# Optimization experiments

Measured on AMD Instinct MI355X. Metric: run time of the kernel, lower is better.

The kernel has to match this reference:

```python
import jax, jax.numpy as jnp
import numpy as np

N, E, G = 50000, 800000, 256
H, C = 8, 16
F0 = 64
FH = H * C  # 128
L = 6
EPS = 1e-5
SEL = [0, 1, 2, 3, 4, 5, 5, 5]  # <10 layers -> pad with last


def setup_inputs() -> dict:
    key = jax.random.key(0)
    ks = jax.random.split(key, 32)

    def w(k, shape, fan_in):
        return jax.random.normal(k, shape, jnp.float32) / np.float32(np.sqrt(fan_in))

    inp = {
        'x': jax.random.normal(ks[0], (N, F0), jnp.float32),
        'edge_index': jax.random.randint(ks[1], (2, E), 0, N),
        'batch_vec': jnp.sort(jax.random.randint(ks[2], (N,), 0, G)),
        # layer 0 (in=F0)
        'Wq0': w(ks[3], (F0, FH), F0), 'bq0': 0.01 * jax.random.normal(ks[4], (FH,), jnp.float32),
        'Wk0': w(ks[5], (F0, FH), F0), 'bk0': 0.01 * jax.random.normal(ks[6], (FH,), jnp.float32),
        'Wv0': w(ks[7], (F0, FH), F0), 'bv0': 0.01 * jax.random.normal(ks[8], (FH,), jnp.float32),
        'Ws0': w(ks[9], (F0, FH), F0), 'bs0': 0.01 * jax.random.normal(ks[10], (FH,), jnp.float32),
        # layers 1..L-1 (in=FH), stacked
        'Wq': w(ks[11], (L - 1, FH, FH), FH), 'bq': 0.01 * jax.random.normal(ks[12], (L - 1, FH), jnp.float32),
        'Wk': w(ks[13], (L - 1, FH, FH), FH), 'bk': 0.01 * jax.random.normal(ks[14], (L - 1, FH), jnp.float32),
        'Wv': w(ks[15], (L - 1, FH, FH), FH), 'bv': 0.01 * jax.random.normal(ks[16], (L - 1, FH), jnp.float32),
        'Ws': w(ks[17], (L - 1, FH, FH), FH), 'bs': 0.01 * jax.random.normal(ks[18], (L - 1, FH), jnp.float32),
        # BatchNorm affine params per layer
        'gamma': jnp.ones((L, FH), jnp.float32),
        'beta': jnp.zeros((L, FH), jnp.float32),
    }
    return inp


def _transformer_conv(x, src, dst, Wq, bq, Wk, bk, Wv, bv, Ws, bs):
    # q from target nodes, k/v from source nodes (PyG TransformerConv, concat=True)
    q = (x @ Wq + bq).reshape(-1, H, C)
    k = (x @ Wk + bk).reshape(-1, H, C)
    v = (x @ Wv + bv).reshape(-1, H, C)
    s = jnp.einsum('ehc,ehc->eh', q[dst], k[src]) * np.float32(1.0 / np.sqrt(C))  # [E,H]
    m = jax.ops.segment_max(s, dst, num_segments=N)       # segment softmax over in-edges
    e = jnp.exp(s - m[dst])
    denom = jax.ops.segment_sum(e, dst, num_segments=N)
    alpha = e / jnp.maximum(denom[dst], 1e-16)            # [E,H]
    msg = jax.ops.segment_sum(alpha[:, :, None] * v[src], dst, num_segments=N)  # [N,H,C]
    return msg.reshape(-1, FH) + (x @ Ws + bs)            # root/skip connection


def _bn_relu(x, g, b):
    mu = jnp.mean(x, axis=0)
    var = jnp.var(x, axis=0)  # biased, as used for normalization in training mode
    return jax.nn.relu((x - mu) * jax.lax.rsqrt(var + EPS) * g + b)


def reference(x, edge_index, batch_vec, Wq0, bq0, Wk0, bk0, Wv0, bv0, Ws0, bs0,
              Wq, bq, Wk, bk, Wv, bv, Ws, bs, gamma, beta):
    src, dst = edge_index[0], edge_index[1]
    outs = []
    h = _bn_relu(_transformer_conv(x, src, dst, Wq0, bq0, Wk0, bk0, Wv0, bv0, Ws0, bs0),
                 gamma[0], beta[0])
    outs.append(h)
    for i in range(L - 1):
        h = _bn_relu(_transformer_conv(h, src, dst, Wq[i], bq[i], Wk[i], bk[i],
                                       Wv[i], bv[i], Ws[i], bs[i]),
                     gamma[i + 1], beta[i + 1])
        outs.append(h)
    counts = jnp.maximum(jax.ops.segment_sum(jnp.ones((N,), x.dtype), batch_vec, num_segments=G), 1.0)
    pooled = [jax.ops.segment_sum(o, batch_vec, num_segments=G) / counts[:, None] for o in outs]
    latent = jnp.stack([pooled[i] for i in SEL], axis=1)  # [G, 8, FH]
    return latent.reshape(G, -1)                          # [G, 8*FH]
```

## Files before the change

### kernel.cpp

```cpp
#include <hip/hip_runtime.h>
#include <hip/hip_bf16.h>
#include <math.h>

#define NN 50000
#define NE 800000
#define NG 256
#define FHH 128
#define NL 6
#define NCH 49
#define NB 391

typedef __attribute__((ext_vector_type(8))) short s16x8;
typedef __attribute__((ext_vector_type(4))) float f32x4;

#define QSCALE 0.36067376022224085f

__device__ __forceinline__ ushort f2bf(float x) {
  uint u = __float_as_uint(x);
  u += 0x7fffu + ((u >> 16) & 1u);
  return (ushort)(u >> 16);
}
__device__ __forceinline__ float bf2f(ushort h) {
  return __uint_as_float(((uint)h) << 16);
}
__device__ __forceinline__ float bfl(uint u) { return __uint_as_float(u << 16); }
__device__ __forceinline__ float bfh(uint u) { return __uint_as_float(u & 0xffff0000u); }

__device__ __forceinline__ void gload16(const ushort* g, ushort* l) {
  __builtin_amdgcn_global_load_lds(
      (const __attribute__((address_space(1))) uint*)(const void*)g,
      (__attribute__((address_space(3))) uint*)(void*)l, 16, 0, 0);
}

__global__ void k_gstart(const int* __restrict__ bv, int* __restrict__ gstart) {
  int g = blockIdx.x * blockDim.x + threadIdx.x;
  if (g > NG) return;
  int lo = 0, hi = NN;
  while (lo < hi) { int mid = (lo + hi) >> 1; if (bv[mid] < g) lo = mid + 1; else hi = mid; }
  gstart[g] = lo;
}

__global__ void k_deg(const int* __restrict__ dstv, int* __restrict__ deg) {
  int e = blockIdx.x * blockDim.x + threadIdx.x;
  if (e < NE) atomicAdd(&deg[dstv[e]], 1);
}

__global__ __launch_bounds__(256) void k_scanA(const int* __restrict__ deg, int* __restrict__ part) {
  int b = blockIdx.x, t = threadIdx.x;
  int s = 0;
  for (int j = t; j < 1024; j += 256) { int i = b * 1024 + j; if (i < NN) s += deg[i]; }
  __shared__ int sh[4];
  for (int o = 32; o; o >>= 1) s += __shfl_down(s, o, 64);
  if ((t & 63) == 0) sh[t >> 6] = s;
  __syncthreads();
  if (t == 0) part[b] = sh[0] + sh[1] + sh[2] + sh[3];
}

__global__ void k_scanB(int* __restrict__ part, int* __restrict__ row_ptr) {
  if (threadIdx.x == 0 && blockIdx.x == 0) {
    int run = 0;
    for (int i = 0; i < NCH; ++i) { int v = part[i]; part[i] = run; run += v; }
    row_ptr[NN] = run;
  }
}

__global__ __launch_bounds__(1024) void k_scanC(const int* __restrict__ deg, const int* __restrict__ part,
                                                int* __restrict__ row_ptr, int* __restrict__ cursor) {
  __shared__ int buf[1024];
  int b = blockIdx.x, t = threadIdx.x;
  int i = b * 1024 + t;
  int v = (i < NN) ? deg[i] : 0;
  buf[t] = v;
  __syncthreads();
  for (int off = 1; off < 1024; off <<= 1) {
    int add = (t >= off) ? buf[t - off] : 0;
    __syncthreads();
    buf[t] += add;
    __syncthreads();
  }
  if (i < NN) { int ex = part[b] + buf[t] - v; row_ptr[i] = ex; cursor[i] = ex; }
}

__global__ void k_scatter(const int* __restrict__ srcv, const int* __restrict__ dstv,
                          int* __restrict__ cursor, uint* __restrict__ colb) {
  int e = blockIdx.x * blockDim.x + threadIdx.x;
  if (e < NE) {
    int d = dstv[e];
    int pos = atomicAdd(&cursor[d], 1);
    colb[pos] = ((uint)srcv[e]) << 9;
  }
}

__device__ __forceinline__ size_t wtile_idx(int k, int c) {
  return (size_t)(k >> 5) * 4096 + ((((c >> 4) * 4 + ((k & 31) >> 3)) * 16 + (c & 15)) * 8 + (k & 7));
}

__global__ __launch_bounds__(256) void k_wconv0(const float* __restrict__ W0, const float* __restrict__ W1,
                                                const float* __restrict__ W2, const float* __restrict__ W3,
                                                ushort* __restrict__ wh, ushort* __restrict__ wl) {
  int id = blockIdx.x * 256 + threadIdx.x;
  if (id >= 4 * 64 * 128) return;
  int mat = id >> 13, rem = id & 8191;
  int k = rem >> 7, c = rem & 127;
  const float* W = (mat == 0) ? W0 : (mat == 1) ? W1 : (mat == 2) ? W2 : W3;
  float v = W[k * 128 + c];
  ushort h = f2bf(v);
  ushort lo = f2bf(v - bf2f(h));
  size_t dst = (size_t)mat * 8192 + wtile_idx(k, c);
  wh[dst] = h; wl[dst] = lo;
}

__global__ __launch_bounds__(256) void k_wconvS(const float* __restrict__ Wq, const float* __restrict__ Wk,
                                                const float* __restrict__ Wv, const float* __restrict__ Ws,
                                                ushort* __restrict__ wh, ushort* __restrict__ wl) {
  int id = blockIdx.x * 256 + threadIdx.x;
  if (id >= 5 * 4 * 16384) return;
  int lay = id / 65536, rem = id % 65536;
  int mat = rem >> 14, rem2 = rem & 16383;
  int k = rem2 >> 7, c = rem2 & 127;
  const float* W = (mat == 0) ? Wq : (mat == 1) ? Wk : (mat == 2) ? Wv : Ws;
  float v = W[(size_t)lay * 16384 + k * 128 + c];
  ushort h = f2bf(v);
  ushort lo = f2bf(v - bf2f(h));
  size_t dst = 32768 + ((size_t)lay * 4 + mat) * 16384 + wtile_idx(k, c);
  wh[dst] = h; wl[dst] = lo;
}

template <int K>
__global__ __launch_bounds__(256) void k_presplit(const float* __restrict__ Y,
                                                  ushort* __restrict__ Xh, ushort* __restrict__ Xl) {
  const int CP = K / 4;
  int idx = blockIdx.x * 256 + threadIdx.x;
  int row = idx / CP;
  int c4 = (idx % CP) * 4;
  if (row >= NN) return;
  float4 v = *reinterpret_cast<const float4*>(Y + (size_t)row * K + c4);
  ushort h0 = f2bf(v.x), h1 = f2bf(v.y), h2 = f2bf(v.z), h3 = f2bf(v.w);
  ushort l0 = f2bf(v.x - bf2f(h0)), l1 = f2bf(v.y - bf2f(h1));
  ushort l2 = f2bf(v.z - bf2f(h2)), l3 = f2bf(v.w - bf2f(h3));
  int b = row >> 7, g = (row & 127) >> 4, frow = row & 15;
  int ks = c4 >> 5, qq = (c4 & 31) >> 3, j = c4 & 7;
  size_t base = ((size_t)ks * NB + b) * 4096 + (((g * 4 + qq) * 16) + frow) * 8 + j;
  *reinterpret_cast<uint2*>(Xh + base) =
      make_uint2((uint)h0 | ((uint)h1 << 16), (uint)h2 | ((uint)h3 << 16));
  *reinterpret_cast<uint2*>(Xl + base) =
      make_uint2((uint)l0 | ((uint)l1 << 16), (uint)l2 | ((uint)l3 << 16));
}

template <int K>
__global__ __launch_bounds__(256, 2) void k_gemm(
    const ushort* __restrict__ Xh, const ushort* __restrict__ Xl,
    const ushort* __restrict__ Wth, const ushort* __restrict__ Wtl,
    const float* __restrict__ b0, const float* __restrict__ b1,
    const float* __restrict__ b2, const float* __restrict__ b3,
    ushort* __restrict__ qbf, ushort* __restrict__ kv, float* __restrict__ Yxs) {
  __shared__ __align__(16) ushort Ah[4096];
  __shared__ __align__(16) ushort Al[4096];
  __shared__ __align__(16) ushort Bh[4096];
  __shared__ __align__(16) ushort Bl[4096];
  int t = threadIdx.x;
  int lane = t & 63, w = t >> 6;
  int wr = w >> 1, wc = w & 1;
  int frow = lane & 15;
  int mat = blockIdx.y;
  const ushort* wh = Wth + (size_t)mat * (K * 128);
  const ushort* wl = Wtl + (size_t)mat * (K * 128);
  const float* bb = (mat == 0) ? b0 : (mat == 1) ? b1 : (mat == 2) ? b2 : b3;

  f32x4 acc[4][4];
#pragma unroll
  for (int i = 0; i < 4; ++i)
#pragma unroll
    for (int j = 0; j < 4; ++j)
#pragma unroll
      for (int r = 0; r < 4; ++r) acc[i][j][r] = 0.f;

  int wofs = w * 1024 + lane * 8;
  for (int ks = 0; ks < K / 32; ++ks) {
    size_t abase = ((size_t)ks * NB + blockIdx.x) * 4096;
    const ushort* gAh = Xh + abase + wofs;
    const ushort* gAl = Xl + abase + wofs;
    const ushort* gBh = wh + ks * 4096 + wofs;
    const ushort* gBl = wl + ks * 4096 + wofs;
    gload16(gAh, &Ah[w * 1024]);
    gload16(gAh + 512, &Ah[w * 1024 + 512]);
    gload16(gAl, &Al[w * 1024]);
    gload16(gAl + 512, &Al[w * 1024 + 512]);
    gload16(gBh, &Bh[w * 1024]);
    gload16(gBh + 512, &Bh[w * 1024 + 512]);
    gload16(gBl, &Bl[w * 1024]);
    gload16(gBl + 512, &Bl[w * 1024 + 512]);
    __syncthreads();
    s16x8 ah[4], al[4], bh[4], bl[4];
#pragma unroll
    for (int g = 0; g < 4; ++g) {
      ah[g] = *reinterpret_cast<const s16x8*>(&Ah[(wr * 4 + g) * 512 + lane * 8]);
      al[g] = *reinterpret_cast<const s16x8*>(&Al[(wr * 4 + g) * 512 + lane * 8]);
      bh[g] = *reinterpret_cast<const s16x8*>(&Bh[(wc * 4 + g) * 512 + lane * 8]);
      bl[g] = *reinterpret_cast<const s16x8*>(&Bl[(wc * 4 + g) * 512 + lane * 8]);
    }
#pragma unroll
    for (int rg = 0; rg < 4; ++rg)
#pragma unroll
      for (int cg = 0; cg < 4; ++cg) {
        acc[rg][cg] = __builtin_amdgcn_mfma_f32_16x16x32_bf16(ah[rg], bh[cg], acc[rg][cg], 0, 0, 0);
        acc[rg][cg] = __builtin_amdgcn_mfma_f32_16x16x32_bf16(al[rg], bh[cg], acc[rg][cg], 0, 0, 0);
        acc[rg][cg] = __builtin_amdgcn_mfma_f32_16x16x32_bf16(ah[rg], bl[cg], acc[rg][cg], 0, 0, 0);
      }
    __syncthreads();
  }
  int r0 = blockIdx.x * 128;
  int qq = (lane >> 4) << 2;
#pragma unroll
  for (int rg = 0; rg < 4; ++rg) {
#pragma unroll
    for (int cg = 0; cg < 4; ++cg) {
      int colg = wc * 64 + cg * 16 + frow;
      float bv = bb[colg];
#pragma unroll
      for (int r = 0; r < 4; ++r) {
        int row = r0 + wr * 64 + rg * 16 + qq + r;
        if (row >= NN) continue;
        float val = acc[rg][cg][r] + bv;
        if (mat == 0)      qbf[(size_t)row * FHH + colg] = f2bf(val * QSCALE);
        else if (mat == 3) Yxs[(size_t)row * FHH + colg] = val;
        else {
          int pos = (colg >> 1) * 4 + ((mat == 2) ? 2 : 0) + (colg & 1);
          kv[(size_t)row * 256 + pos] = f2bf(val);
        }
      }
    }
  }
}

__global__ __launch_bounds__(256) void k_agg(const uint* __restrict__ qb,
                                             const ushort* __restrict__ kv,
                                             const float* __restrict__ xs,
                                             const int* __restrict__ row_ptr,
                                             const uint* __restrict__ colb,
                                             float* __restrict__ y) {
  int n = blockIdx.x * 4 + (threadIdx.x >> 6);
  int t = threadIdx.x & 63;
  uint qp = qb[(n << 6) + t];
  float qx = bfl(qp), qy = bfh(qp);
  const char* kvb = (const char*)kv;
  uint tof = (uint)t * 8u;
  int e0 = row_ptr[n], e1 = row_ptr[n + 1];
  float sum = 0.f, a0 = 0.f, a1 = 0.f;
  int i = e0;
  for (; i + 4 <= e1; i += 4) {
    uint o0 = colb[i] + tof, o1 = colb[i + 1] + tof;
    uint o2 = colb[i + 2] + tof, o3 = colb[i + 3] + tof;
    uint2 d0 = *(const uint2*)(kvb + o0);
    uint2 d1 = *(const uint2*)(kvb + o1);
    uint2 d2 = *(const uint2*)(kvb + o2);
    uint2 d3 = *(const uint2*)(kvb + o3);
    float p0 = fmaf(qx, bfl(d0.x), qy * bfh(d0.x));
    float p1 = fmaf(qx, bfl(d1.x), qy * bfh(d1.x));
    float p2 = fmaf(qx, bfl(d2.x), qy * bfh(d2.x));
    float p3 = fmaf(qx, bfl(d3.x), qy * bfh(d3.x));
    p0 += __shfl_xor(p0, 1, 8); p1 += __shfl_xor(p1, 1, 8);
    p2 += __shfl_xor(p2, 1, 8); p3 += __shfl_xor(p3, 1, 8);
    p0 += __shfl_xor(p0, 2, 8); p1 += __shfl_xor(p1, 2, 8);
    p2 += __shfl_xor(p2, 2, 8); p3 += __shfl_xor(p3, 2, 8);
    p0 += __shfl_xor(p0, 4, 8); p1 += __shfl_xor(p1, 4, 8);
    p2 += __shfl_xor(p2, 4, 8); p3 += __shfl_xor(p3, 4, 8);
    float w0 = exp2f(fminf(p0, 110.f));
    float w1 = exp2f(fminf(p1, 110.f));
    float w2 = exp2f(fminf(p2, 110.f));
    float w3 = exp2f(fminf(p3, 110.f));
    sum += (w0 + w1) + (w2 + w3);
    a0 = fmaf(w0, bfl(d0.y), fmaf(w1, bfl(d1.y), fmaf(w2, bfl(d2.y), fmaf(w3, bfl(d3.y), a0))));
    a1 = fmaf(w0, bfh(d0.y), fmaf(w1, bfh(d1.y), fmaf(w2, bfh(d2.y), fmaf(w3, bfh(d3.y), a1))));
  }
  for (; i < e1; ++i) {
    uint o0 = colb[i] + tof;
    uint2 d0 = *(const uint2*)(kvb + o0);
    float p0 = fmaf(qx, bfl(d0.x), qy * bfh(d0.x));
    p0 += __shfl_xor(p0, 1, 8);
    p0 += __shfl_xor(p0, 2, 8);
    p0 += __shfl_xor(p0, 4, 8);
    float w0 = exp2f(fminf(p0, 110.f));
    sum += w0;
    a0 = fmaf(w0, bfl(d0.y), a0);
    a1 = fmaf(w0, bfh(d0.y), a1);
  }
  float inv = 1.f / fmaxf(sum, 1e-16f);
  float2 xv = *reinterpret_cast<const float2*>(xs + ((size_t)n << 7) + 2 * t);
  float2 ov;
  ov.x = fmaf(a0, inv, xv.x);
  ov.y = fmaf(a1, inv, xv.y);
  *reinterpret_cast<float2*>(y + ((size_t)n << 7) + 2 * t) = ov;
}

__global__ __launch_bounds__(256) void k_bnstats(const float* __restrict__ y,
                                                 float* __restrict__ sums,
                                                 float* __restrict__ sumsq) {
  __shared__ float s1[256], s2[256];
  int f = threadIdx.x & 127;
  int half = threadIdx.x >> 7;
  float a = 0.f, b = 0.f;
  for (int r = blockIdx.x * 2 + half; r < NN; r += 512) {
    float val = y[(size_t)r * FHH + f];
    a += val;
    b += val * val;
  }
  s1[threadIdx.x] = a;
  s2[threadIdx.x] = b;
  __syncthreads();
  if (half == 0) {
    a += s1[threadIdx.x + 128];
    b += s2[threadIdx.x + 128];
    atomicAdd(&sums[f], a);
    atomicAdd(&sumsq[f], b);
  }
}

template <int WRITE_X>
__global__ __launch_bounds__(256) void k_post(const float* __restrict__ y,
                                              const float* __restrict__ sums,
                                              const float* __restrict__ sumsq,
                                              const float* __restrict__ gvec,
                                              const float* __restrict__ bvec_,
                                              const int* __restrict__ bv,
                                              const int* __restrict__ gstart,
                                              float* __restrict__ out, int layer,
                                              ushort* __restrict__ Xh, ushort* __restrict__ Xl) {
  __shared__ float acts[8][128];
  __shared__ int sg[8];
  __shared__ float ssc[128], ssh[128];
  int b = blockIdx.x, t = threadIdx.x;
  if (t < 128) {
    const float invn = 1.f / (float)NN;
    float mu = sums[t] * invn;
    float var = sumsq[t] * invn - mu * mu;
    float sc = gvec[t] * rsqrtf(var + 1e-5f);
    ssc[t] = sc;
    ssh[t] = bvec_[t] - mu * sc;
  }
  if (t < 8) sg[t] = (b * 8 + t < NN) ? bv[b * 8 + t] : -1;
  __syncthreads();
  int row = b * 8 + (t >> 5);
  int c4 = (t & 31) * 4;
  bool ok = row < NN;
  float4 a = make_float4(0.f, 0.f, 0.f, 0.f);
  if (ok) {
    float4 v = *reinterpret_cast<const float4*>(y + (size_t)row * FHH + c4);
    a.x = fmaxf(fmaf(v.x, ssc[c4 + 0], ssh[c4 + 0]), 0.f);
    a.y = fmaxf(fmaf(v.y, ssc[c4 + 1], ssh[c4 + 1]), 0.f);
    a.z = fmaxf(fmaf(v.z, ssc[c4 + 2], ssh[c4 + 2]), 0.f);
    a.w = fmaxf(fmaf(v.w, ssc[c4 + 3], ssh[c4 + 3]), 0.f);
  }
  *reinterpret_cast<float4*>(&acts[t >> 5][c4]) = a;
  if (WRITE_X && ok) {
    ushort h0 = f2bf(a.x), h1 = f2bf(a.y), h2 = f2bf(a.z), h3 = f2bf(a.w);
    ushort l0 = f2bf(a.x - bf2f(h0)), l1 = f2bf(a.y - bf2f(h1));
    ushort l2 = f2bf(a.z - bf2f(h2)), l3 = f2bf(a.w - bf2f(h3));
    int bb = row >> 7, g = (row & 127) >> 4, frow = row & 15;
    int ks = c4 >> 5, qq = (c4 & 31) >> 3, j = c4 & 7;
    size_t base = ((size_t)ks * NB + bb) * 4096 + (((g * 4 + qq) * 16) + frow) * 8 + j;
    *reinterpret_cast<uint2*>(Xh + base) =
        make_uint2((uint)h0 | ((uint)h1 << 16), (uint)h2 | ((uint)h3 << 16));
    *reinterpret_cast<uint2*>(Xl + base) =
        make_uint2((uint)l0 | ((uint)l1 << 16), (uint)l2 | ((uint)l3 << 16));
  }
  __syncthreads();
  if (t < 128) {
    float racc = 0.f;
    int cg = sg[0];
    for (int r = 0; r < 8; ++r) {
      int g = sg[r];
      if (g != cg) {
        if (cg >= 0) {
          float p = racc / (float)(gstart[cg + 1] - gstart[cg]);
          if (layer < 5) atomicAdd(&out[(size_t)cg * 1024 + layer * FHH + t], p);
          else {
            atomicAdd(&out[(size_t)cg * 1024 + 5 * FHH + t], p);
            atomicAdd(&out[(size_t)cg * 1024 + 6 * FHH + t], p);
            atomicAdd(&out[(size_t)cg * 1024 + 7 * FHH + t], p);
          }
        }
        racc = 0.f;
        cg = g;
      }
      racc += acts[r][t];
    }
    if (cg >= 0) {
      float p = racc / (float)(gstart[cg + 1] - gstart[cg]);
      if (layer < 5) atomicAdd(&out[(size_t)cg * 1024 + layer * FHH + t], p);
      else {
        atomicAdd(&out[(size_t)cg * 1024 + 5 * FHH + t], p);
        atomicAdd(&out[(size_t)cg * 1024 + 6 * FHH + t], p);
        atomicAdd(&out[(size_t)cg * 1024 + 7 * FHH + t], p);
      }
    }
  }
}

extern "C" void kernel_launch(void* const* d_in, const int* in_sizes, int n_in,
                              void* d_out, int out_size, void* d_ws, size_t ws_size,
                              hipStream_t stream) {
  (void)in_sizes; (void)n_in; (void)ws_size;
  const float* x    = (const float*)d_in[0];
  const int*   ei   = (const int*)d_in[1];
  const int*   bvec = (const int*)d_in[2];
  const float* Wq0  = (const float*)d_in[3];
  const float* bq0  = (const float*)d_in[4];
  const float* Wk0  = (const float*)d_in[5];
  const float* bk0  = (const float*)d_in[6];
  const float* Wv0  = (const float*)d_in[7];
  const float* bv0  = (const float*)d_in[8];
  const float* Ws0  = (const float*)d_in[9];
  const float* bs0  = (const float*)d_in[10];
  const float* WqS  = (const float*)d_in[11];
  const float* bqS  = (const float*)d_in[12];
  const float* WkS  = (const float*)d_in[13];
  const float* bkS  = (const float*)d_in[14];
  const float* WvS  = (const float*)d_in[15];
  const float* bvS  = (const float*)d_in[16];
  const float* WsS  = (const float*)d_in[17];
  const float* bsS  = (const float*)d_in[18];
  const float* gamma = (const float*)d_in[19];
  const float* beta  = (const float*)d_in[20];
  float* out = (float*)d_out;

  char* ws = (char*)d_ws;
  size_t off = 0;
  auto alloc = [&](size_t bytes) {
    void* p = ws + off;
    off = (off + bytes + 255) & ~(size_t)255;
    return p;
  };
  ushort* qbf = (ushort*)alloc((size_t)NN * FHH * 2);
  float* xs   = (float*)alloc((size_t)NN * FHH * 4);
  float* y    = (float*)alloc((size_t)NN * FHH * 4);
  ushort* kv  = (ushort*)alloc((size_t)NN * 256 * 2);
  ushort* Xh  = (ushort*)alloc((size_t)4 * NB * 4096 * 2 + 8192);
  ushort* Xl  = (ushort*)alloc((size_t)4 * NB * 4096 * 2 + 8192);
  uint* colb   = (uint*)alloc((size_t)NE * 4);
  int* row_ptr = (int*)alloc((size_t)(NN + 1) * 4);
  int* cursor  = (int*)alloc((size_t)NN * 4);
  int* deg     = (int*)alloc((size_t)NN * 4);
  int* part    = (int*)alloc((size_t)NCH * 4);
  int* gstart  = (int*)alloc((size_t)(NG + 1) * 4);
  float* bstat = (float*)alloc((size_t)NL * 2 * FHH * 4);
  ushort* wsh = (ushort*)alloc((size_t)360448 * 2);
  ushort* wsl = (ushort*)alloc((size_t)360448 * 2);

  const int* srcv = ei;
  const int* dstv = ei + NE;

  hipMemsetAsync(out, 0, (size_t)out_size * 4, stream);
  hipMemsetAsync(deg, 0, (size_t)NN * 4, stream);
  hipMemsetAsync(bstat, 0, (size_t)NL * 2 * FHH * 4, stream);
  k_gstart<<<5, 64, 0, stream>>>(bvec, gstart);
  k_deg<<<(NE + 255) / 256, 256, 0, stream>>>(dstv, deg);
  k_scanA<<<NCH, 256, 0, stream>>>(deg, part);
  k_scanB<<<1, 64, 0, stream>>>(part, row_ptr);
  k_scanC<<<NCH, 1024, 0, stream>>>(deg, part, row_ptr, cursor);
  k_scatter<<<(NE + 255) / 256, 256, 0, stream>>>(srcv, dstv, cursor, colb);
  k_wconv0<<<128, 256, 0, stream>>>(Wq0, Wk0, Wv0, Ws0, wsh, wsl);
  k_wconvS<<<1280, 256, 0, stream>>>(WqS, WkS, WvS, WsS, wsh, wsl);
  k_presplit<64><<<(NN * 16 + 255) / 256, 256, 0, stream>>>(x, Xh, Xl);

  for (int l = 0; l < NL; ++l) {
    const ushort* WthL = wsh + ((l == 0) ? 0 : (size_t)32768 + (size_t)(l - 1) * 65536);
    const ushort* WtlL = wsl + ((l == 0) ? 0 : (size_t)32768 + (size_t)(l - 1) * 65536);
    const float *bq_, *bk_, *bv_, *bs_;
    if (l == 0) { bq_ = bq0; bk_ = bk0; bv_ = bv0; bs_ = bs0; }
    else {
      size_t bo = (size_t)(l - 1) * FHH;
      bq_ = bqS + bo; bk_ = bkS + bo; bv_ = bvS + bo; bs_ = bsS + bo;
    }
    dim3 gg(NB, 4);
    if (l == 0)
      k_gemm<64><<<gg, 256, 0, stream>>>(Xh, Xl, WthL, WtlL, bq_, bk_, bv_, bs_, qbf, kv, xs);
    else
      k_gemm<128><<<gg, 256, 0, stream>>>(Xh, Xl, WthL, WtlL, bq_, bk_, bv_, bs_, qbf, kv, xs);
    k_agg<<<NN / 4, 256, 0, stream>>>((const uint*)qbf, kv, xs, row_ptr, colb, y);
    float* lsum = bstat + (size_t)l * 2 * FHH;
    float* lsqs = lsum + FHH;
    k_bnstats<<<256, 256, 0, stream>>>(y, lsum, lsqs);
    if (l + 1 < NL)
      k_post<1><<<6250, 256, 0, stream>>>(y, lsum, lsqs, gamma + (size_t)l * FHH,
                                          beta + (size_t)l * FHH, bvec, gstart, out, l, Xh, Xl);
    else
      k_post<0><<<6250, 256, 0, stream>>>(y, lsum, lsqs, gamma + (size_t)l * FHH,
                                          beta + (size_t)l * FHH, bvec, gstart, out, l, Xh, Xl);
  }
}
```

Before: 1.019 ms.

## Fuse BatchNorm statistics into aggregation kernel and remap GEMM grid for locality

The separate k_bnstats pass over y is removed. k_agg now reduces each block's per-feature sum and sum of squares in shared memory and atomically adds them into 8 striped partial buffers, which k_post sums before computing the scale and shift. The GEMM launch is flattened to a 1D grid in which 8 consecutive row-blocks share each weight matrix, grouped across the four matrices, so the A tiles are reused from cache. This saves one full read of y per layer. In exchange it adds 6250 blocks' worth of atomics per layer and some early-exiting GEMM blocks.

```diff
diff --git a/kernel.cpp b/kernel.cpp
--- a/kernel.cpp
+++ b/kernel.cpp
@@ -158,11 +158,14 @@
   __shared__ __align__(16) ushort Al[4096];
   __shared__ __align__(16) ushort Bh[4096];
   __shared__ __align__(16) ushort Bl[4096];
+  int bid = blockIdx.x;
+  int mat = (bid >> 3) & 3;
+  int b = (bid & 7) + ((bid >> 5) << 3);
+  if (b >= NB) return;
   int t = threadIdx.x;
   int lane = t & 63, w = t >> 6;
   int wr = w >> 1, wc = w & 1;
   int frow = lane & 15;
-  int mat = blockIdx.y;
   const ushort* wh = Wth + (size_t)mat * (K * 128);
   const ushort* wl = Wtl + (size_t)mat * (K * 128);
   const float* bb = (mat == 0) ? b0 : (mat == 1) ? b1 : (mat == 2) ? b2 : b3;
@@ -177,7 +180,7 @@
 
   int wofs = w * 1024 + lane * 8;
   for (int ks = 0; ks < K / 32; ++ks) {
-    size_t abase = ((size_t)ks * NB + blockIdx.x) * 4096;
+    size_t abase = ((size_t)ks * NB + b) * 4096;
     const ushort* gAh = Xh + abase + wofs;
     const ushort* gAl = Xl + abase + wofs;
     const ushort* gBh = wh + ks * 4096 + wofs;
@@ -209,7 +212,7 @@
       }
     __syncthreads();
   }
-  int r0 = blockIdx.x * 128;
+  int r0 = b * 128;
   int qq = (lane >> 4) << 2;
 #pragma unroll
   for (int rg = 0; rg < 4; ++rg) {
@@ -238,8 +241,12 @@
                                              const float* __restrict__ xs,
                                              const int* __restrict__ row_ptr,
                                              const uint* __restrict__ colb,
-                                             float* __restrict__ y) {
-  int n = blockIdx.x * 4 + (threadIdx.x >> 6);
+                                             float* __restrict__ y,
+                                             float* __restrict__ stats) {
+  __shared__ float2 red[4][64];
+  __shared__ float2 red2[4][64];
+  int wv = threadIdx.x >> 6;
+  int n = blockIdx.x * 4 + wv;
   int t = threadIdx.x & 63;
   uint qp = qb[(n << 6) + t];
   float qx = bfl(qp), qy = bfh(qp);
@@ -291,35 +298,26 @@
   ov.x = fmaf(a0, inv, xv.x);
   ov.y = fmaf(a1, inv, xv.y);
   *reinterpret_cast<float2*>(y + ((size_t)n << 7) + 2 * t) = ov;
-}
-
-__global__ __launch_bounds__(256) void k_bnstats(const float* __restrict__ y,
-                                                 float* __restrict__ sums,
-                                                 float* __restrict__ sumsq) {
-  __shared__ float s1[256], s2[256];
-  int f = threadIdx.x & 127;
-  int half = threadIdx.x >> 7;
-  float a = 0.f, b = 0.f;
-  for (int r = blockIdx.x * 2 + half; r < NN; r += 512) {
-    float val = y[(size_t)r * FHH + f];
-    a += val;
-    b += val * val;
-  }
-  s1[threadIdx.x] = a;
-  s2[threadIdx.x] = b;
+  red[wv][t] = ov;
+  red2[wv][t] = make_float2(ov.x * ov.x, ov.y * ov.y);
   __syncthreads();
-  if (half == 0) {
-    a += s1[threadIdx.x + 128];
-    b += s2[threadIdx.x + 128];
-    atomicAdd(&sums[f], a);
-    atomicAdd(&sumsq[f], b);
+  if (threadIdx.x < 64) {
+    float2 s = red[0][t], q2 = red2[0][t];
+    s.x += red[1][t].x + red[2][t].x + red[3][t].x;
+    s.y += red[1][t].y + red[2][t].y + red[3][t].y;
+    q2.x += red2[1][t].x + red2[2][t].x + red2[3][t].x;
+    q2.y += red2[1][t].y + red2[2][t].y + red2[3][t].y;
+    float* st = stats + (blockIdx.x & 7) * 256;
+    atomicAdd(st + 2 * t, s.x);
+    atomicAdd(st + 2 * t + 1, s.y);
+    atomicAdd(st + 128 + 2 * t, q2.x);
+    atomicAdd(st + 128 + 2 * t + 1, q2.y);
   }
 }
 
 template <int WRITE_X>
 __global__ __launch_bounds__(256) void k_post(const float* __restrict__ y,
-                                              const float* __restrict__ sums,
-                                              const float* __restrict__ sumsq,
+                                              const float* __restrict__ st,
                                               const float* __restrict__ gvec,
                                               const float* __restrict__ bvec_,
                                               const int* __restrict__ bv,
@@ -331,9 +329,12 @@
   __shared__ float ssc[128], ssh[128];
   int b = blockIdx.x, t = threadIdx.x;
   if (t < 128) {
+    float s = 0.f, q = 0.f;
+#pragma unroll
+    for (int c = 0; c < 8; ++c) { s += st[c * 256 + t]; q += st[c * 256 + 128 + t]; }
     const float invn = 1.f / (float)NN;
-    float mu = sums[t] * invn;
-    float var = sumsq[t] * invn - mu * mu;
+    float mu = s * invn;
+    float var = q * invn - mu * mu;
     float sc = gvec[t] * rsqrtf(var + 1e-5f);
     ssc[t] = sc;
     ssh[t] = bvec_[t] - mu * sc;
@@ -443,7 +444,7 @@
   int* deg     = (int*)alloc((size_t)NN * 4);
   int* part    = (int*)alloc((size_t)NCH * 4);
   int* gstart  = (int*)alloc((size_t)(NG + 1) * 4);
-  float* bstat = (float*)alloc((size_t)NL * 2 * FHH * 4);
+  float* bstat = (float*)alloc((size_t)NL * 8 * 256 * 4);
   ushort* wsh = (ushort*)alloc((size_t)360448 * 2);
   ushort* wsl = (ushort*)alloc((size_t)360448 * 2);
 
@@ -452,7 +453,7 @@
 
   hipMemsetAsync(out, 0, (size_t)out_size * 4, stream);
   hipMemsetAsync(deg, 0, (size_t)NN * 4, stream);
-  hipMemsetAsync(bstat, 0, (size_t)NL * 2 * FHH * 4, stream);
+  hipMemsetAsync(bstat, 0, (size_t)NL * 8 * 256 * 4, stream);
   k_gstart<<<5, 64, 0, stream>>>(bvec, gstart);
   k_deg<<<(NE + 255) / 256, 256, 0, stream>>>(dstv, deg);
   k_scanA<<<NCH, 256, 0, stream>>>(deg, part);
@@ -463,6 +464,7 @@
   k_wconvS<<<1280, 256, 0, stream>>>(WqS, WkS, WvS, WsS, wsh, wsl);
   k_presplit<64><<<(NN * 16 + 255) / 256, 256, 0, stream>>>(x, Xh, Xl);
 
+  const int GEMM_GRID = 49 * 32;
   for (int l = 0; l < NL; ++l) {
     const ushort* WthL = wsh + ((l == 0) ? 0 : (size_t)32768 + (size_t)(l - 1) * 65536);
     const ushort* WtlL = wsl + ((l == 0) ? 0 : (size_t)32768 + (size_t)(l - 1) * 65536);
@@ -472,20 +474,17 @@
       size_t bo = (size_t)(l - 1) * FHH;
       bq_ = bqS + bo; bk_ = bkS + bo; bv_ = bvS + bo; bs_ = bsS + bo;
     }
-    dim3 gg(NB, 4);
     if (l == 0)
-      k_gemm<64><<<gg, 256, 0, stream>>>(Xh, Xl, WthL, WtlL, bq_, bk_, bv_, bs_, qbf, kv, xs);
+      k_gemm<64><<<GEMM_GRID, 256, 0, stream>>>(Xh, Xl, WthL, WtlL, bq_, bk_, bv_, bs_, qbf, kv, xs);
     else
-      k_gemm<128><<<gg, 256, 0, stream>>>(Xh, Xl, WthL, WtlL, bq_, bk_, bv_, bs_, qbf, kv, xs);
-    k_agg<<<NN / 4, 256, 0, stream>>>((const uint*)qbf, kv, xs, row_ptr, colb, y);
-    float* lsum = bstat + (size_t)l * 2 * FHH;
-    float* lsqs = lsum + FHH;
-    k_bnstats<<<256, 256, 0, stream>>>(y, lsum, lsqs);
+      k_gemm<128><<<GEMM_GRID, 256, 0, stream>>>(Xh, Xl, WthL, WtlL, bq_, bk_, bv_, bs_, qbf, kv, xs);
+    float* lstat = bstat + (size_t)l * 8 * 256;
+    k_agg<<<NN / 4, 256, 0, stream>>>((const uint*)qbf, kv, xs, row_ptr, colb, y, lstat);
     if (l + 1 < NL)
-      k_post<1><<<6250, 256, 0, stream>>>(y, lsum, lsqs, gamma + (size_t)l * FHH,
+      k_post<1><<<6250, 256, 0, stream>>>(y, lstat, gamma + (size_t)l * FHH,
                                           beta + (size_t)l * FHH, bvec, gstart, out, l, Xh, Xl);
     else
-      k_post<0><<<6250, 256, 0, stream>>>(y, lsum, lsqs, gamma + (size_t)l * FHH,
+      k_post<0><<<6250, 256, 0, stream>>>(y, lstat, gamma + (size_t)l * FHH,
                                           beta + (size_t)l * FHH, bvec, gstart, out, l, Xh, Xl);
   }
 }
```

Measured after the change: 1.033 ms. Within noise of the previous version (+1.3%).
